# Optimization experiments

Hardware: AMD Instinct MI355X
Metric: run time of the kernel (lower is better)

The kernel has to match this reference:

```python
import jax, jax.numpy as jnp
import numpy as np

# ---- static configuration (from init_kwargs) ----
L = 36.0            # cubic cell edge (bohr)
G = 180             # grid points per axis
NA = 64             # number of atoms
NRAD = 8            # basis['n']
NL = 4              # basis['l']
RO = 2.5            # basis['r_o'] (bohr)
A = L / G           # grid spacing (orthorhombic -> U = diag(A))
RMAX = int(np.ceil(RO / A))          # half-width of periodic box (13)
B = 2 * RMAX + 1                     # box edge (27)
VCELL = A ** 3                       # |det U|
# static coefficient mask: keep (n,l,m) with |m - NL| <= l  (same as tril*flip(tril))
_MASK = np.abs(np.arange(2 * NL + 1)[None, :] - NL) <= np.arange(NL)[:, None]


def _make_W():
    # orthonormalization matrix W = S^{-1/2} for radials phi_n(r) = r^2 (r_o - r)^{n+2}
    r = np.linspace(0.0, RO, 4000)
    phi = np.stack([r ** 2 * (RO - r) ** (n + 2) for n in range(NRAD)])
    S = np.trapz(phi[:, None] * phi[None, :], r, axis=-1)
    w, v = np.linalg.eigh(S)
    return (v @ np.diag(w ** -0.5) @ v.T).astype(np.float32)


def setup_inputs() -> dict:
    key = jax.random.key(0)
    k1, k2 = jax.random.split(key)
    rho = jax.random.uniform(k1, (G, G, G), dtype=jnp.float32)       # electron density >= 0
    positions = jax.random.uniform(k2, (NA, 3), dtype=jnp.float32) * L
    return {"rho": rho, "positions": positions, "W": jnp.asarray(_make_W())}


def _sph_padded(theta, phi):
    # real spherical harmonics, zero-padded to [NL, 2*NL+1, ...] with m at index NL+m
    ct = jnp.cos(theta); st = jnp.sin(theta)
    cp = jnp.cos(phi); sp = jnp.sin(phi)
    c2p = jnp.cos(2 * phi); s2p = jnp.sin(2 * phi)
    c3p = jnp.cos(3 * phi); s3p = jnp.sin(3 * phi)
    z = jnp.zeros_like(theta)
    one = jnp.ones_like(theta)
    Y = {
        (0, 0): 0.28209479177387814 * one,
        (1, -1): 0.4886025119029199 * st * sp,
        (1, 0): 0.4886025119029199 * ct,
        (1, 1): 0.4886025119029199 * st * cp,
        (2, -2): 0.5462742152960396 * st ** 2 * s2p,
        (2, -1): 1.0925484305920792 * st * ct * sp,
        (2, 0): 0.31539156525252005 * (3 * ct ** 2 - 1),
        (2, 1): 1.0925484305920792 * st * ct * cp,
        (2, 2): 0.5462742152960396 * st ** 2 * c2p,
        (3, -3): 0.5900435899266435 * st ** 3 * s3p,
        (3, -2): 1.445305721320277 * st ** 2 * ct * s2p,
        (3, -1): 0.4570457994644658 * st * (5 * ct ** 2 - 1) * sp,
        (3, 0): 0.3731763325901154 * (5 * ct ** 3 - 3 * ct),
        (3, 1): 0.4570457994644658 * st * (5 * ct ** 2 - 1) * cp,
        (3, 2): 1.445305721320277 * st ** 2 * ct * c2p,
        (3, 3): 0.5900435899266435 * st ** 3 * c3p,
    }
    rows = []
    for l in range(NL):
        pad = [z] * (NL - l)
        rows.append(jnp.stack(pad + [Y[(l, m)] for m in range(-l, l + 1)] + pad))
    return jnp.stack(rows)  # [NL, 2NL+1, B, B, B]


def _project_atom(rho, pos, W):
    a = jnp.float32(A)
    cm = jnp.round(pos / a)            # nearest grid index of atom (U_inv @ pos)
    dr = pos - a * cm                  # sub-grid displacement
    offs = jnp.arange(-RMAX, RMAX + 1, dtype=jnp.float32)
    # periodic mesh indices (box_around / fmod wrap)
    Xm = jnp.mod(offs + cm[0], G).astype(jnp.int32)
    Ym = jnp.mod(offs + cm[1], G).astype(jnp.int32)
    Zm = jnp.mod(offs + cm[2], G).astype(jnp.int32)
    srho = rho[Xm[:, None, None], Ym[None, :, None], Zm[None, None, :]]  # [B,B,B] gather
    # euclidean coords relative to the atom
    Xs = (offs * a - dr[0])[:, None, None]
    Ys = (offs * a - dr[1])[None, :, None]
    Zs = (offs * a - dr[2])[None, None, :]
    Xs, Ys, Zs = jnp.broadcast_arrays(Xs, Ys, Zs)
    R = jnp.sqrt(Xs ** 2 + Ys ** 2 + Zs ** 2)
    Rsafe = jnp.where(R < 1e-12, 1.0, R)
    Theta = jnp.where(R < 1e-12, 0.0, jnp.arccos(jnp.clip(Zs / Rsafe, -1.0, 1.0)))
    Phi = jnp.arctan2(Ys, Xs)
    angs = _sph_padded(Theta, Phi)                       # [NL, 2NL+1, B,B,B]
    ns = jnp.arange(NRAD, dtype=jnp.float32)[:, None, None, None]
    phi_n = jnp.where(R < RO, R ** 2 * jnp.maximum(RO - R, 0.0) ** (ns + 2.0), 0.0)
    rads = jnp.einsum('nm,mijk->nijk', W, phi_n) * jnp.float32(VCELL)  # [NRAD, B,B,B]
    coeff = jnp.einsum('lmijk,nijk,ijk->nlm', angs, rads, srho)        # [NRAD, NL, 2NL+1]
    return coeff[:, _MASK].reshape(-1)                    # [NRAD * NL^2] = 128


def reference(rho, positions, W):
    # vmap over atoms (single species -> identical box shape per atom)
    return jax.vmap(lambda p: _project_atom(rho, p, W))(positions)  # [NA, 128]
```

## Files before the change

kernel.cpp:

```cpp
#include <hip/hip_runtime.h>

#define G 180
#define NRAD 8
#define RO_F 2.5f
#define A_F 0.2f
#define VCELL_F 0.008f
#define CELLS 19683
#define SLABS 16
#define NATOMS 64
#define ITERS 10


__global__ __launch_bounds__(256, 3) void proj_kernel(
    const float* __restrict__ rho, const float* __restrict__ pos,
    float* __restrict__ ws)
{
    const int atom = blockIdx.y;
    const int slab = blockIdx.x;
    const int tid  = threadIdx.x;
    const int lane = tid & 63;
    const int w    = tid >> 6;
    const int g    = w >> 1;
    const int cw   = w & 1;

    const float px = pos[atom*3+0], py = pos[atom*3+1], pz = pos[atom*3+2];
    const float cmx = rintf(px * 5.0f), cmy = rintf(py * 5.0f), cmz = rintf(pz * 5.0f);
    const float drx = px - A_F*cmx, dry = py - A_F*cmy, drz = pz - A_F*cmz;
    const int icx = (int)cmx - 13, icy = (int)cmy - 13, icz = (int)cmz - 13;

    float acc[64];
    #pragma unroll
    for (int j = 0; j < 64; ++j) acc[j] = 0.0f;

    int c = slab*128 + cw*64 + lane;

    int i_n, j_n, k_n; float s_n;
    {
        int i = c / 729; int rem = c - i*729; int j = rem / 27; int k = rem - j*27;
        int gx = i + icx; gx += (gx < 0) ? G : 0; gx -= (gx >= G) ? G : 0;
        int gy = j + icy; gy += (gy < 0) ? G : 0; gy -= (gy >= G) ? G : 0;
        int gz = k + icz; gz += (gz < 0) ? G : 0; gz -= (gz >= G) ? G : 0;
        i_n = i; j_n = j; k_n = k;
        s_n = rho[(gx*G + gy)*G + gz];
    }

    for (int it = 0; it < ITERS; ++it) {
        const int i = i_n, j = j_n, k = k_n;
        const float s = s_n;
        c += SLABS*128;
        if (it != ITERS-1) {
            int i2 = c / 729; int rem = c - i2*729; int j2 = rem / 27; int k2 = rem - j2*27;
            int gx = i2 + icx; gx += (gx < 0) ? G : 0; gx -= (gx >= G) ? G : 0;
            int gy = j2 + icy; gy += (gy < 0) ? G : 0; gy -= (gy >= G) ? G : 0;
            int gz = k2 + icz; gz += (gz < 0) ? G : 0; gz -= (gz >= G) ? G : 0;
            i_n = i2; j_n = j2; k_n = k2;
            s_n = rho[(gx*G + gy)*G + gz];
        }

        float x = (float)(i-13)*A_F - drx;
        float y = (float)(j-13)*A_F - dry;
        float z = (float)(k-13)*A_F - drz;
        float r2 = x*x + y*y + z*z;
        float inv = rsqrtf(fmaxf(r2, 1e-24f));
        float R = r2 * inv;
        if (R < RO_F) {
            float t = RO_F - R;
            float ux = x*inv, uy = y*inv, uz = z*inv;
            float uz2 = uz*uz;
            float ux2 = ux*ux, uy2 = uy*uy;
            float ys[16];
            ys[0]  = 0.28209479177f;
            ys[1]  = 0.48860251190f * uy;
            ys[2]  = 0.48860251190f * uz;
            ys[3]  = 0.48860251190f * ux;
            ys[4]  = 1.09254843059f * ux*uy;
            ys[5]  = 1.09254843059f * uy*uz;
            ys[6]  = 0.31539156525f * (3.0f*uz2 - 1.0f);
            ys[7]  = 1.09254843059f * ux*uz;
            ys[8]  = 0.54627421530f * (ux2 - uy2);
            ys[9]  = 0.59004358993f * uy*(3.0f*ux2 - uy2);
            ys[10] = 2.89061144264f * ux*uy*uz;
            ys[11] = 0.45704579946f * uy*(5.0f*uz2 - 1.0f);
            ys[12] = 0.37317633259f * uz*(5.0f*uz2 - 3.0f);
            ys[13] = 0.45704579946f * ux*(5.0f*uz2 - 1.0f);
            ys[14] = 1.44530572132f * (ux2 - uy2)*uz;
            ys[15] = 0.59004358993f * ux*(ux2 - 3.0f*uy2);

            float t2 = t*t;
            float p0 = s * r2 * t2;
            if (g) { float t4 = t2*t2; p0 *= t4; }
            float p1 = p0*t, p2 = p1*t, p3 = p2*t;
            #pragma unroll
            for (int q = 0; q < 16; ++q) {
                acc[q]    = fmaf(p0, ys[q], acc[q]);
                acc[16+q] = fmaf(p1, ys[q], acc[16+q]);
                acc[32+q] = fmaf(p2, ys[q], acc[32+q]);
                acc[48+q] = fmaf(p3, ys[q], acc[48+q]);
            }
        }
    }

    __shared__ float red[4][64][33];
    __shared__ float stage[4][2][32];
    const int col  = lane & 31;
    const int half = lane >> 5;
    #pragma unroll
    for (int ch = 0; ch < 2; ++ch) {
        #pragma unroll
        for (int q = 0; q < 32; ++q)
            red[w][lane][q] = acc[ch*32 + q];
        float csum = 0.0f;
        #pragma unroll
        for (int r = 0; r < 32; ++r)
            csum += red[w][half*32 + r][col];
        stage[w][half][col] = csum;
        if (lane < 32) {
            float v = stage[w][0][lane] + stage[w][1][lane];
            ws[((atom*SLABS + slab)*4 + w)*64 + ch*32 + lane] = v;
        }
    }
}

__global__ void finalize_kernel(const float* __restrict__ ws,
                                const float* __restrict__ W,
                                float* __restrict__ out)
{
    const int atom = blockIdx.x;
    const int t = threadIdx.x;
    const int n = t >> 4, q = t & 15;
    const int g = n >> 2, r = n & 3;
    const float* base = ws + atom*SLABS*4*64;
    float m = 0.0f;
    #pragma unroll
    for (int s = 0; s < SLABS; ++s) {
        m += base[(s*4 + g*2 + 0)*64 + r*16 + q];
        m += base[(s*4 + g*2 + 1)*64 + r*16 + q];
    }
    __shared__ float M[8][16];
    M[n][q] = m;
    __syncthreads();
    float sum = 0.0f;
    #pragma unroll
    for (int k = 0; k < 8; ++k)
        sum = fmaf(W[n*8+k], M[k][q], sum);
    out[atom*128 + t] = sum * VCELL_F;
}

extern "C" void kernel_launch(void* const* d_in, const int* in_sizes, int n_in,
                              void* d_out, int out_size, void* d_ws, size_t ws_size,
                              hipStream_t stream) {
    const float* rho = (const float*)d_in[0];
    const float* pos = (const float*)d_in[1];
    const float* W   = (const float*)d_in[2];
    float* out = (float*)d_out;
    float* ws  = (float*)d_ws;

    dim3 grid(SLABS, NATOMS);
    proj_kernel<<<grid, 256, 0, stream>>>(rho, pos, ws);
    finalize_kernel<<<NATOMS, 128, 0, stream>>>(ws, W, out);
}
```

Before: 80.23 us.

## Pack accumulators into float2 FMAs, use incremental indexing, shuffle-based reduction

The 64 scalar accumulators and the spherical harmonic values are packed into two-wide float vectors, so the compiler can emit packed FP32 FMAs (v_pk_fma_f32) and halve the FMA instruction count in the inner loop. The per-iteration integer divisions used to turn the cell index into (i,j,k) are replaced by incremental carry arithmetic, since the stride of 2048 cells maps to a fixed (2,21,23) step. The final cross-half reduction uses a wave shuffle instead of a shared-memory stage array. Packed math may change register allocation and the vector pairing constraints can add move instructions.

New measurement: 79.06 us. About the same (-1.4%).

```diff
diff --git a/kernel.cpp b/kernel.cpp
--- a/kernel.cpp
+++ b/kernel.cpp
@@ -9,6 +9,8 @@
 #define SLABS 16
 #define NATOMS 64
 #define ITERS 10
+
+typedef float float2v __attribute__((ext_vector_type(2)));
 
 
 __global__ __launch_bounds__(256, 3) void proj_kernel(
@@ -28,32 +30,37 @@
     const float drx = px - A_F*cmx, dry = py - A_F*cmy, drz = pz - A_F*cmz;
     const int icx = (int)cmx - 13, icy = (int)cmy - 13, icz = (int)cmz - 13;
 
-    float acc[64];
+    float2v acc2[32];
     #pragma unroll
-    for (int j = 0; j < 64; ++j) acc[j] = 0.0f;
+    for (int j = 0; j < 32; ++j) acc2[j] = (float2v){0.0f, 0.0f};
 
-    int c = slab*128 + cw*64 + lane;
+    const int c0 = slab*128 + cw*64 + lane;
+    int i_n = c0 / 729;
+    int rem = c0 - i_n*729;
+    int j_n = rem / 27;
+    int k_n = rem - j_n*27;
 
-    int i_n, j_n, k_n; float s_n;
+    float s_n;
     {
-        int i = c / 729; int rem = c - i*729; int j = rem / 27; int k = rem - j*27;
-        int gx = i + icx; gx += (gx < 0) ? G : 0; gx -= (gx >= G) ? G : 0;
-        int gy = j + icy; gy += (gy < 0) ? G : 0; gy -= (gy >= G) ? G : 0;
-        int gz = k + icz; gz += (gz < 0) ? G : 0; gz -= (gz >= G) ? G : 0;
-        i_n = i; j_n = j; k_n = k;
+        int gx = i_n + icx; gx += (gx < 0) ? G : 0; gx -= (gx >= G) ? G : 0;
+        int gy = j_n + icy; gy += (gy < 0) ? G : 0; gy -= (gy >= G) ? G : 0;
+        int gz = k_n + icz; gz += (gz < 0) ? G : 0; gz -= (gz >= G) ? G : 0;
         s_n = rho[(gx*G + gy)*G + gz];
     }
 
     for (int it = 0; it < ITERS; ++it) {
         const int i = i_n, j = j_n, k = k_n;
         const float s = s_n;
-        c += SLABS*128;
         if (it != ITERS-1) {
-            int i2 = c / 729; int rem = c - i2*729; int j2 = rem / 27; int k2 = rem - j2*27;
-            int gx = i2 + icx; gx += (gx < 0) ? G : 0; gx -= (gx >= G) ? G : 0;
-            int gy = j2 + icy; gy += (gy < 0) ? G : 0; gy -= (gy >= G) ? G : 0;
-            int gz = k2 + icz; gz += (gz < 0) ? G : 0; gz -= (gz >= G) ? G : 0;
-            i_n = i2; j_n = j2; k_n = k2;
+            int kk = k_n + 23, jc = 0;
+            if (kk >= 27) { kk -= 27; jc = 1; }
+            int jj = j_n + 21 + jc, ic = 0;
+            if (jj >= 27) { jj -= 27; ic = 1; }
+            int ii = i_n + 2 + ic;
+            i_n = ii; j_n = jj; k_n = kk;
+            int gx = ii + icx; gx += (gx < 0) ? G : 0; gx -= (gx >= G) ? G : 0;
+            int gy = jj + icy; gy += (gy < 0) ? G : 0; gy -= (gy >= G) ? G : 0;
+            int gz = kk + icz; gz += (gz < 0) ? G : 0; gz -= (gz >= G) ? G : 0;
             s_n = rho[(gx*G + gy)*G + gz];
         }
 
@@ -68,56 +75,57 @@
             float ux = x*inv, uy = y*inv, uz = z*inv;
             float uz2 = uz*uz;
             float ux2 = ux*ux, uy2 = uy*uy;
-            float ys[16];
-            ys[0]  = 0.28209479177f;
-            ys[1]  = 0.48860251190f * uy;
-            ys[2]  = 0.48860251190f * uz;
-            ys[3]  = 0.48860251190f * ux;
-            ys[4]  = 1.09254843059f * ux*uy;
-            ys[5]  = 1.09254843059f * uy*uz;
-            ys[6]  = 0.31539156525f * (3.0f*uz2 - 1.0f);
-            ys[7]  = 1.09254843059f * ux*uz;
-            ys[8]  = 0.54627421530f * (ux2 - uy2);
-            ys[9]  = 0.59004358993f * uy*(3.0f*ux2 - uy2);
-            ys[10] = 2.89061144264f * ux*uy*uz;
-            ys[11] = 0.45704579946f * uy*(5.0f*uz2 - 1.0f);
-            ys[12] = 0.37317633259f * uz*(5.0f*uz2 - 3.0f);
-            ys[13] = 0.45704579946f * ux*(5.0f*uz2 - 1.0f);
-            ys[14] = 1.44530572132f * (ux2 - uy2)*uz;
-            ys[15] = 0.59004358993f * ux*(ux2 - 3.0f*uy2);
+            float2v ys2[8];
+            ys2[0] = (float2v){0.28209479177f,
+                               0.48860251190f * uy};
+            ys2[1] = (float2v){0.48860251190f * uz,
+                               0.48860251190f * ux};
+            ys2[2] = (float2v){1.09254843059f * ux*uy,
+                               1.09254843059f * uy*uz};
+            ys2[3] = (float2v){0.31539156525f * (3.0f*uz2 - 1.0f),
+                               1.09254843059f * ux*uz};
+            ys2[4] = (float2v){0.54627421530f * (ux2 - uy2),
+                               0.59004358993f * uy*(3.0f*ux2 - uy2)};
+            ys2[5] = (float2v){2.89061144264f * ux*uy*uz,
+                               0.45704579946f * uy*(5.0f*uz2 - 1.0f)};
+            ys2[6] = (float2v){0.37317633259f * uz*(5.0f*uz2 - 3.0f),
+                               0.45704579946f * ux*(5.0f*uz2 - 1.0f)};
+            ys2[7] = (float2v){1.44530572132f * (ux2 - uy2)*uz,
+                               0.59004358993f * ux*(ux2 - 3.0f*uy2)};
 
             float t2 = t*t;
             float p0 = s * r2 * t2;
             if (g) { float t4 = t2*t2; p0 *= t4; }
             float p1 = p0*t, p2 = p1*t, p3 = p2*t;
+            float2v vp0 = (float2v){p0, p0};
+            float2v vp1 = (float2v){p1, p1};
+            float2v vp2 = (float2v){p2, p2};
+            float2v vp3 = (float2v){p3, p3};
             #pragma unroll
-            for (int q = 0; q < 16; ++q) {
-                acc[q]    = fmaf(p0, ys[q], acc[q]);
-                acc[16+q] = fmaf(p1, ys[q], acc[16+q]);
-                acc[32+q] = fmaf(p2, ys[q], acc[32+q]);
-                acc[48+q] = fmaf(p3, ys[q], acc[48+q]);
+            for (int q8 = 0; q8 < 8; ++q8) {
+                acc2[q8]      = vp0 * ys2[q8] + acc2[q8];
+                acc2[8  + q8] = vp1 * ys2[q8] + acc2[8  + q8];
+                acc2[16 + q8] = vp2 * ys2[q8] + acc2[16 + q8];
+                acc2[24 + q8] = vp3 * ys2[q8] + acc2[24 + q8];
             }
         }
     }
 
     __shared__ float red[4][64][33];
-    __shared__ float stage[4][2][32];
     const int col  = lane & 31;
     const int half = lane >> 5;
     #pragma unroll
     for (int ch = 0; ch < 2; ++ch) {
         #pragma unroll
         for (int q = 0; q < 32; ++q)
-            red[w][lane][q] = acc[ch*32 + q];
+            red[w][lane][q] = acc2[(ch*32 + q) >> 1][q & 1];
         float csum = 0.0f;
         #pragma unroll
         for (int r = 0; r < 32; ++r)
             csum += red[w][half*32 + r][col];
-        stage[w][half][col] = csum;
-        if (lane < 32) {
-            float v = stage[w][0][lane] + stage[w][1][lane];
-            ws[((atom*SLABS + slab)*4 + w)*64 + ch*32 + lane] = v;
-        }
+        float other = __shfl_down(csum, 32);
+        if (lane < 32)
+            ws[((atom*SLABS + slab)*4 + w)*64 + ch*32 + lane] = csum + other;
     }
 }
 
```
